# Kernel tuning notes

Measured on AMD Instinct MI355X. Metric: run time of the kernel, lower is better.

The kernel has to match this reference:

```python
import jax, jax.numpy as jnp
import numpy as np

PHI = 1.6
JITTER = 1e-4
ETA = 1.0
BETA = 0.5
EPS_CHOL = 1e-6
R_NEIGH = 2


def _solve3(L, d):
    # lower-triangular 3x3 forward substitution; L broadcasts against d[..., 3]
    y0 = d[..., 0] / L[..., 0, 0]
    y1 = (d[..., 1] - L[..., 1, 0] * y0) / L[..., 1, 1]
    y2 = (d[..., 2] - L[..., 2, 0] * y0 - L[..., 2, 1] * y1) / L[..., 2, 2]
    return jnp.stack([y0, y1, y2], axis=-1)


def _overlap_score(delta, L):
    # fused_gaussian_overlap_score: Gaussian log-overlap ~ -0.5*(Mahalanobis + logdet)
    y = _solve3(L, delta)
    maha = jnp.sum(y * y, axis=-1)
    logdet = 2.0 * jnp.sum(jnp.log(jnp.diagonal(L, axis1=-2, axis2=-1)), axis=-1)
    return -0.5 * (maha + logdet)


def _head(x, ln_g, ln_b, W1, b1, W2, b2):
    # LayerNorm -> Linear -> SiLU -> Linear(->1), squeeze
    m = jnp.mean(x, axis=-1, keepdims=True)
    v = jnp.var(x, axis=-1, keepdims=True)
    h = (x - m) / jnp.sqrt(v + 1e-5) * ln_g + ln_b
    h = jax.nn.silu(h @ W1 + b1)
    return (h @ W2 + b2)[..., 0]


def setup_inputs() -> dict:
    key = jax.random.key(0)
    ks = jax.random.split(key, 12)
    B, Kp, M, C = 2, 1024, 8, 256
    s_parent = jax.random.normal(ks[0], (B, Kp, C), jnp.float32)
    mu_p = jax.random.normal(ks[1], (B, Kp, 3), jnp.float32) * 10.0
    A = jax.random.normal(ks[2], (B, Kp, 3, 3), jnp.float32) * 0.5
    Sigma_p = jnp.einsum('bkij,bklj->bkil', A, A) + 0.05 * jnp.eye(3, dtype=jnp.float32)
    mask_parent = jnp.ones((B, Kp), jnp.float32)
    xi_noise = jax.random.normal(ks[3], (B, Kp, M, 3), jnp.float32)
    emb = jax.random.normal(ks[4], (M, C), jnp.float32) * 0.02
    lin = lambda k, fi, fo, s=0.02: jax.random.normal(k, (fi, fo), jnp.float32) * s
    return dict(
        s_parent=s_parent, mu_p=mu_p, Sigma_p=Sigma_p, mask_parent=mask_parent,
        xi_noise=xi_noise, emb=emb,
        gate_ln_g=jnp.ones((C,), jnp.float32), gate_ln_b=jnp.zeros((C,), jnp.float32),
        gate_W1=lin(ks[5], C, C), gate_b1=jnp.zeros((C,), jnp.float32),
        gate_W2=lin(ks[6], C, 1), gate_b2=jnp.zeros((1,), jnp.float32),
        prior_ln_g=jnp.ones((C,), jnp.float32), prior_ln_b=jnp.zeros((C,), jnp.float32),
        prior_W1=lin(ks[7], C, C), prior_b1=jnp.zeros((C,), jnp.float32),
        prior_W2=lin(ks[8], C, 1), prior_b2=jnp.zeros((1,), jnp.float32),
        geom_W=lin(ks[9], C, 3, 0.01), geom_b=jnp.zeros((3,), jnp.float32),
        K_target=6144,
    )


def reference(s_parent, mu_p, Sigma_p, mask_parent, xi_noise, emb,
              gate_ln_g, gate_ln_b, gate_W1, gate_b1, gate_W2, gate_b2,
              prior_ln_g, prior_ln_b, prior_W1, prior_b1, prior_W2, prior_b2,
              geom_W, geom_b, K_target):
    B, Kp, C = s_parent.shape
    M = emb.shape[0]
    Kc = Kp * M
    I3 = jnp.eye(3, dtype=s_parent.dtype)

    # --- candidate children from per-parent Cholesky splat ---
    Lp = jnp.linalg.cholesky(Sigma_p + EPS_CHOL * I3)               # [B,Kp,3,3]
    xi = xi_noise + (emb @ geom_W + geom_b)                          # [B,Kp,M,3]
    mu0 = mu_p[:, :, None, :] + jnp.einsum('bkae,bkme->bkma', Lp, xi)
    mu0 = mu0.reshape(B, Kc, 3)

    j0 = jnp.repeat(jnp.arange(Kp), M)                               # [Kc] birth parent
    t_ids = jnp.tile(jnp.arange(M), Kp)                              # [Kc] child slot
    m0 = mask_parent[:, j0]

    # --- gate g ---
    gate_in = s_parent[:, j0, :] + emb[t_ids]                        # [B,Kc,C]
    b = _head(gate_in, gate_ln_g, gate_ln_b, gate_W1, gate_b1, gate_W2, gate_b2)
    a = jax.nn.softplus(_head(s_parent, prior_ln_g, prior_ln_b, prior_W1, prior_b1, prior_W2, prior_b2))
    b = b + BETA * jnp.log(a[:, j0] + 1e-8)
    g = jax.nn.sigmoid(b / max(ETA, 1e-6)) * m0                      # [B,Kc]
    loss_count = jnp.mean((jnp.sum(g, axis=1) - float(K_target)) ** 2)

    # --- top-R neighbor parents by overlap score (indices only, no grad) ---
    mu0_birth = mu_p[:, j0, :]                                       # mu of birth parent
    delta1 = mu0_birth[:, :, None, :] - mu_p[:, None, :, :]          # [B,Kc,Kp,3]
    score1 = _overlap_score(delta1, Lp[:, None])                     # [B,Kc,Kp]
    self_hot = (jnp.arange(Kp)[None, :] == j0[:, None])              # [Kc,Kp]
    score1 = jnp.where(self_hot[None], 1e9, score1)
    _, neigh = jax.lax.top_k(jax.lax.stop_gradient(score1), R_NEIGH) # [B,Kc,R], col0=j0

    bidx = jnp.arange(B)[:, None, None]
    mu_nei = mu_p[bidx, neigh]                                       # [B,Kc,R,3]
    Sig_nei = Sigma_p[bidx, neigh]                                   # [B,Kc,R,3,3]
    L_nei = Lp[bidx, neigh]
    s_nei = s_parent[bidx, neigh]                                    # [B,Kc,R,C]

    # --- soft responsibilities over the R neighbors ---
    score2 = _overlap_score(mu0[:, :, None, :] - mu_nei, L_nei)      # [B,Kc,R]
    w = jax.nn.softmax(score2, axis=-1)

    # --- moment-matching refine (sparse form of B_resp: rows of B are w scattered at neigh) ---
    mu_child = jnp.einsum('bir,bird->bid', w, mu_nei)                # [B,Kc,3]
    intra = jnp.einsum('bir,birmn->bimn', w, Sig_nei) * PHI ** (-2)
    dmu = mu_nei - mu_child[:, :, None, :]
    inter = jnp.einsum('bir,birm,birn->bimn', w, dmu, dmu)
    Sigma_child = intra + inter + JITTER * I3                        # [B,Kc,3,3]

    s_mix = jnp.einsum('bir,birc->bic', w, s_nei)
    s_child0 = g[..., None] * s_mix                                  # [B,Kc,C]
    return s_child0, mu_child, Sigma_child, g, loss_count
```

## Files before the change

### kernel.cpp

```cpp
#include <hip/hip_runtime.h>
#include <math.h>

#define NPAR 2048
#define KP   1024
#define MM   8
#define CC   256
#define KC   8192
#define NCH  16384

#define WS_PKL    0
#define WS_PKI    8192
#define WS_PKM    16384
#define WS_L22    24576
#define WS_MEANSP 26624
#define WS_SUMSQ  28672
#define WS_DOT8   30720
#define WS_APRIOR 47104
#define WS_EGATE  49152
#define WS_UGATE  51200
#define WS_C0GATE 51456
#define WS_GEO    51712
#define WS_MEANE  51736
#define WS_SUMSQE 51744
#define WS_NEIGH  51752
#define WS_PGATE  53824

#define OUT_S    0
#define OUT_MU   4194304
#define OUT_SIG  4243456
#define OUT_G    4390912
#define OUT_LOSS 4407296

__device__ __forceinline__ float siluf(float x){ return x / (1.f + expf(-x)); }
__device__ __forceinline__ float softplusf(float x){ return x > 20.f ? x : log1pf(expf(x)); }

__global__ __launch_bounds__(256) void kP1(const float* __restrict__ sp,
                                           const float* __restrict__ mu_p,
                                           const float* __restrict__ Sig,
                                           const float* __restrict__ emb,
                                           const float* __restrict__ geom_W,
                                           const float* __restrict__ geom_b,
                                           float* __restrict__ ws) {
  int blk = blockIdx.x;
  int t = threadIdx.x;
  if (blk < 512) {
    int pid  = blk * 4 + (t >> 6);
    int lane = t & 63;
    const float4 v = *(const float4*)(sp + pid * CC + lane * 4);
    float s  = v.x + v.y + v.z + v.w;
    float ss = v.x*v.x + v.y*v.y + v.z*v.z + v.w*v.w;
    float pd[8];
#pragma unroll
    for (int m = 0; m < 8; m++) {
      float4 e = *(const float4*)(emb + m * CC + lane * 4);
      pd[m] = v.x*e.x + v.y*e.y + v.z*e.z + v.w*e.w;
    }
#pragma unroll
    for (int o = 32; o > 0; o >>= 1) {
      s  += __shfl_xor(s, o);
      ss += __shfl_xor(ss, o);
#pragma unroll
      for (int m = 0; m < 8; m++) pd[m] += __shfl_xor(pd[m], o);
    }
    if (lane == 0) {
      ws[WS_MEANSP + pid] = s * (1.f / 256.f);
      ws[WS_SUMSQ + pid]  = ss;
#pragma unroll
      for (int m = 0; m < 8; m++) ws[WS_DOT8 + pid * 8 + m] = pd[m];
    }
  } else if (blk < 520) {
    int pid = (blk - 512) * 256 + t;
    const float* S = Sig + pid * 9;
    float a00 = S[0] + 1e-6f, a10 = S[3], a11 = S[4] + 1e-6f;
    float a20 = S[6], a21 = S[7], a22 = S[8] + 1e-6f;
    float L00 = sqrtf(a00); float i0 = 1.f / L00;
    float L10 = a10 * i0, L20 = a20 * i0;
    float L11 = sqrtf(a11 - L10 * L10); float i1 = 1.f / L11;
    float L21 = (a21 - L20 * L10) * i1;
    float L22 = sqrtf(a22 - L20 * L20 - L21 * L21); float i2 = 1.f / L22;
    float logdet = 2.f * logf(L00 * L11 * L22);
    float4 pkl = {L10, L20, L21, logdet};
    float4 pki = {i0, i1, i2, L00};
    float4 pkm = {mu_p[pid*3+0], mu_p[pid*3+1], mu_p[pid*3+2], L11};
    *(float4*)(ws + WS_PKL + pid * 4) = pkl;
    *(float4*)(ws + WS_PKI + pid * 4) = pki;
    *(float4*)(ws + WS_PKM + pid * 4) = pkm;
    ws[WS_L22 + pid] = L22;
  } else {
    if (t < 192) {
      int o = t >> 3, lane8 = t & 7;
      int m = o / 3, d = o % 3;
      float acc = 0.f;
      for (int k = lane8; k < 256; k += 8) acc += emb[m * 256 + k] * geom_W[k * 3 + d];
      acc += __shfl_xor(acc, 1); acc += __shfl_xor(acc, 2); acc += __shfl_xor(acc, 4);
      if (lane8 == 0) ws[WS_GEO + o] = acc + geom_b[d];
    } else {
      int o = (t - 192) >> 3, lane8 = t & 7;
      if (o < 8) {
        float s = 0.f, ss = 0.f;
        for (int k = lane8; k < 256; k += 8) { float e = emb[o * 256 + k]; s += e; ss += e * e; }
        s  += __shfl_xor(s, 1);  s  += __shfl_xor(s, 2);  s  += __shfl_xor(s, 4);
        ss += __shfl_xor(ss, 1); ss += __shfl_xor(ss, 2); ss += __shfl_xor(ss, 4);
        if (lane8 == 0) { ws[WS_MEANE + o] = s * (1.f / 256.f); ws[WS_SUMSQE + o] = ss; }
      }
    }
  }
}

__global__ __launch_bounds__(256) void kP2(const float* __restrict__ sp,
                                           const float* __restrict__ emb,
                                           const float* __restrict__ g_ln_g,
                                           const float* __restrict__ g_ln_b,
                                           const float* __restrict__ gW1,
                                           const float* __restrict__ gb1,
                                           const float* __restrict__ p_ln_g,
                                           const float* __restrict__ p_ln_b,
                                           const float* __restrict__ pW1,
                                           const float* __restrict__ pb1,
                                           const float* __restrict__ pW2,
                                           const float* __restrict__ pb2,
                                           float* __restrict__ ws) {
  __shared__ float xs[8][256];
  __shared__ float red[4][8];
  __shared__ float redS[4][8];
  __shared__ float redQ[4][8];
  __shared__ float mv[2][8];
  int blk = blockIdx.x;
  int t = threadIdx.x;

  if (blk < 512) {
    int wv = blk * 4 + (t >> 6);
    int lane = t & 63;
    int b = wv >> 10;
    int j = wv & (KP - 1);
    const float4 qm = *(const float4*)(ws + WS_PKM + wv * 4);
    float qx = qm.x, qy = qm.y, qz = qm.z;
    float best = -3.4e38f; int bidx = 1 << 30;
    for (int it = 0; it < 16; it++) {
      int k = it * 64 + lane;
      int idx = b * KP + k;
      float4 pl = *(const float4*)(ws + WS_PKL + idx * 4);
      float4 pi = *(const float4*)(ws + WS_PKI + idx * 4);
      float4 pm = *(const float4*)(ws + WS_PKM + idx * 4);
      float dx = qx - pm.x, dy = qy - pm.y, dz = qz - pm.z;
      float y0 = dx * pi.x;
      float y1 = (dy - pl.x * y0) * pi.y;
      float y2 = (dz - pl.y * y0 - pl.z * y1) * pi.z;
      float sc = -0.5f * (y0*y0 + y1*y1 + y2*y2 + pl.w);
      if (k == j) sc = -3.4e38f;
      if (sc > best || (sc == best && k < bidx)) { best = sc; bidx = k; }
    }
#pragma unroll
    for (int o = 32; o > 0; o >>= 1) {
      float ob = __shfl_xor(best, o);
      int   oi = __shfl_xor(bidx, o);
      if (ob > best || (ob == best && oi < bidx)) { best = ob; bidx = oi; }
    }
    if (lane == 0) ((int*)ws)[WS_NEIGH + wv] = bidx;
  } else {
    int cblk = blk - 512;
    bool prior = (cblk >= 256 && cblk < 512);
    const float* W1 = prior ? pW1 : gW1;

    if (cblk < 256) {
      int base = cblk * 8;
      float g = g_ln_g[t];
#pragma unroll
      for (int r = 0; r < 8; r++) xs[r][t] = sp[(base + r) * 256 + t] * g;
    } else if (cblk < 512) {
      int base = (cblk - 256) * 8;
      float vr[8], s1[8], s2[8];
#pragma unroll
      for (int r = 0; r < 8; r++) {
        vr[r] = sp[(base + r) * 256 + t];
        s1[r] = vr[r];
        s2[r] = vr[r] * vr[r];
      }
#pragma unroll
      for (int o = 32; o > 0; o >>= 1) {
#pragma unroll
        for (int r = 0; r < 8; r++) { s1[r] += __shfl_xor(s1[r], o); s2[r] += __shfl_xor(s2[r], o); }
      }
      int wave = t >> 6;
      if ((t & 63) == 0) {
#pragma unroll
        for (int r = 0; r < 8; r++) { redS[wave][r] = s1[r]; redQ[wave][r] = s2[r]; }
      }
      __syncthreads();
      if (t < 8) {
        float sum = redS[0][t] + redS[1][t] + redS[2][t] + redS[3][t];
        float sq  = redQ[0][t] + redQ[1][t] + redQ[2][t] + redQ[3][t];
        float mean = sum * (1.f / 256.f);
        float var  = sq * (1.f / 256.f) - mean * mean;
        mv[0][t] = mean;
        mv[1][t] = rsqrtf(var + 1e-5f);
      }
      __syncthreads();
      float pg = p_ln_g[t], pbv = p_ln_b[t];
#pragma unroll
      for (int r = 0; r < 8; r++)
        xs[r][t] = (vr[r] - mv[0][r]) * mv[1][r] * pg + pbv;
    } else if (cblk == 512) {
      float g = g_ln_g[t];
#pragma unroll
      for (int r = 0; r < 8; r++) xs[r][t] = emb[r * 256 + t] * g;
    } else {
      xs[0][t] = g_ln_g[t];
      xs[1][t] = g_ln_b[t];
#pragma unroll
      for (int r = 2; r < 8; r++) xs[r][t] = 0.f;
    }
    __syncthreads();

    float acc[8] = {0,0,0,0,0,0,0,0};
    for (int k4 = 0; k4 < 256; k4 += 4) {
      float w0 = W1[(k4+0) * 256 + t];
      float w1 = W1[(k4+1) * 256 + t];
      float w2 = W1[(k4+2) * 256 + t];
      float w3 = W1[(k4+3) * 256 + t];
#pragma unroll
      for (int r = 0; r < 8; r++) {
        float4 x4 = *(const float4*)&xs[r][k4];
        acc[r] += x4.x * w0 + x4.y * w1 + x4.z * w2 + x4.w * w3;
      }
    }

    if (cblk < 256) {
      int base = cblk * 8;
#pragma unroll
      for (int r = 0; r < 8; r++) ws[WS_PGATE + (base + r) * 256 + t] = acc[r];
    } else if (cblk < 512) {
      int base = (cblk - 256) * 8;
      float b1 = pb1[t], w2 = pW2[t];
      float tv[8];
#pragma unroll
      for (int r = 0; r < 8; r++) {
        float h = acc[r] + b1;
        tv[r] = siluf(h) * w2;
      }
#pragma unroll
      for (int o = 32; o > 0; o >>= 1) {
#pragma unroll
        for (int r = 0; r < 8; r++) tv[r] += __shfl_xor(tv[r], o);
      }
      int wave = t >> 6;
      if ((t & 63) == 0) {
#pragma unroll
        for (int r = 0; r < 8; r++) red[wave][r] = tv[r];
      }
      __syncthreads();
      if (t < 8) {
        float sum = red[0][t] + red[1][t] + red[2][t] + red[3][t] + pb2[0];
        ws[WS_APRIOR + base + t] = softplusf(sum);
      }
    } else if (cblk == 512) {
#pragma unroll
      for (int r = 0; r < 8; r++) ws[WS_EGATE + r * 256 + t] = acc[r];
    } else {
      ws[WS_UGATE + t]  = acc[0];
      ws[WS_C0GATE + t] = acc[1] + gb1[t];
    }
  }
}

__global__ __launch_bounds__(256) void kD(const float* __restrict__ sp,
                                          const float* __restrict__ Sig,
                                          const float* __restrict__ mask,
                                          const float* __restrict__ xi_noise,
                                          const float* __restrict__ gW2,
                                          const float* __restrict__ gb2,
                                          const float* __restrict__ ws,
                                          float* __restrict__ out) {
  int wv   = blockIdx.x * 4 + (threadIdx.x >> 6);
  int lane = threadIdx.x & 63;
  int b = wv >> 13;
  int i = wv & (KC - 1);
  int j = i >> 3;
  int m = i & 7;
  int prow = b * KP + j;

  float mean_x = ws[WS_MEANSP + prow] + ws[WS_MEANE + m];
  float Ex2 = ws[WS_SUMSQ + prow] + 2.f * ws[WS_DOT8 + prow * 8 + m] + ws[WS_SUMSQE + m];
  float var = Ex2 * (1.f / 256.f) - mean_x * mean_x;
  float rstd = rsqrtf(var + 1e-5f);

  int c4 = lane * 4;
  float Pv[4], Ev[4], Uv[4], C0v[4], W2v[4];
  *(float4*)Pv  = *(const float4*)(ws + WS_PGATE + prow * 256 + c4);
  *(float4*)Ev  = *(const float4*)(ws + WS_EGATE + m * 256 + c4);
  *(float4*)Uv  = *(const float4*)(ws + WS_UGATE + c4);
  *(float4*)C0v = *(const float4*)(ws + WS_C0GATE + c4);
  *(float4*)W2v = *(const float4*)(gW2 + c4);
  float partial = 0.f;
#pragma unroll
  for (int q = 0; q < 4; q++) {
    float pre = (Pv[q] + Ev[q] - mean_x * Uv[q]) * rstd + C0v[q];
    partial += siluf(pre) * W2v[q];
  }
#pragma unroll
  for (int o = 32; o > 0; o >>= 1) partial += __shfl_xor(partial, o);
  float aP = ws[WS_APRIOR + prow];
  float bval = partial + gb2[0] + 0.5f * logf(aP + 1e-8f);
  float g = (1.f / (1.f + expf(-bval))) * mask[prow];

  const float4 plP = *(const float4*)(ws + WS_PKL + prow * 4);
  const float4 piP = *(const float4*)(ws + WS_PKI + prow * 4);
  const float4 pmP = *(const float4*)(ws + WS_PKM + prow * 4);
  float L22 = ws[WS_L22 + prow];

  int xbase = (prow * 8 + m) * 3;
  float x0 = xi_noise[xbase + 0] + ws[WS_GEO + m * 3 + 0];
  float x1 = xi_noise[xbase + 1] + ws[WS_GEO + m * 3 + 1];
  float x2 = xi_noise[xbase + 2] + ws[WS_GEO + m * 3 + 2];
  float m0x = pmP.x + piP.w * x0;
  float m0y = pmP.y + plP.x * x0 + pmP.w * x1;
  float m0z = pmP.z + plP.y * x0 + plP.z * x1 + L22 * x2;

  int n1 = ((const int*)ws)[WS_NEIGH + prow];
  int nrow1 = b * KP + n1;
  const float4 plN = *(const float4*)(ws + WS_PKL + nrow1 * 4);
  const float4 piN = *(const float4*)(ws + WS_PKI + nrow1 * 4);
  const float4 pmN = *(const float4*)(ws + WS_PKM + nrow1 * 4);

  float sc[2], nx[2], ny[2], nz[2];
  {
    float dx = m0x - pmP.x, dy = m0y - pmP.y, dz = m0z - pmP.z;
    float y0 = dx * piP.x;
    float y1 = (dy - plP.x * y0) * piP.y;
    float y2 = (dz - plP.y * y0 - plP.z * y1) * piP.z;
    sc[0] = -0.5f * (y0*y0 + y1*y1 + y2*y2 + plP.w);
    nx[0] = pmP.x; ny[0] = pmP.y; nz[0] = pmP.z;
  }
  {
    float dx = m0x - pmN.x, dy = m0y - pmN.y, dz = m0z - pmN.z;
    float y0 = dx * piN.x;
    float y1 = (dy - plN.x * y0) * piN.y;
    float y2 = (dz - plN.y * y0 - plN.z * y1) * piN.z;
    sc[1] = -0.5f * (y0*y0 + y1*y1 + y2*y2 + plN.w);
    nx[1] = pmN.x; ny[1] = pmN.y; nz[1] = pmN.z;
  }
  float mxs = fmaxf(sc[0], sc[1]);
  float e0 = expf(sc[0] - mxs), e1 = expf(sc[1] - mxs);
  float inv = 1.f / (e0 + e1);
  float w0 = e0 * inv, w1 = e1 * inv;

  float mcx = w0 * nx[0] + w1 * nx[1];
  float mcy = w0 * ny[0] + w1 * ny[1];
  float mcz = w0 * nz[0] + w1 * nz[1];

  float d0x = nx[0] - mcx, d0y = ny[0] - mcy, d0z = nz[0] - mcz;
  float d1x = nx[1] - mcx, d1y = ny[1] - mcy, d1z = nz[1] - mcz;
  const float* S0 = Sig + prow * 9;
  const float* S1 = Sig + nrow1 * 9;
  const float PHIm2 = 0.390625f;
  float Sout[9];
  float dd0[3] = {d0x, d0y, d0z};
  float dd1[3] = {d1x, d1y, d1z};
#pragma unroll
  for (int a = 0; a < 3; a++)
#pragma unroll
    for (int e = 0; e < 3; e++) {
      float v = (w0 * S0[a*3+e] + w1 * S1[a*3+e]) * PHIm2
              + w0 * dd0[a] * dd0[e] + w1 * dd1[a] * dd1[e];
      if (a == e) v += 1e-4f;
      Sout[a*3+e] = v;
    }

  if (lane == 0) {
    float* om = out + OUT_MU + wv * 3;
    om[0] = mcx; om[1] = mcy; om[2] = mcz;
    out[OUT_G + wv] = g;
    float* os = out + OUT_SIG + wv * 9;
#pragma unroll
    for (int q = 0; q < 9; q++) os[q] = Sout[q];
  }

  float s0v[4], s1v[4], ov[4];
  *(float4*)s0v = *(const float4*)(sp + prow * 256 + c4);
  *(float4*)s1v = *(const float4*)(sp + nrow1 * 256 + c4);
  float gw0 = g * w0, gw1 = g * w1;
#pragma unroll
  for (int q = 0; q < 4; q++) ov[q] = gw0 * s0v[q] + gw1 * s1v[q];
  *(float4*)(out + OUT_S + wv * 256 + c4) = *(float4*)ov;
}

__global__ __launch_bounds__(256) void kF(const float* __restrict__ out_in,
                                          const int* __restrict__ Kt,
                                          float* __restrict__ out) {
  __shared__ float red[4][2];
  int t = threadIdx.x;
  const float* gp = out_in + OUT_G;
  float s0 = 0.f, s1 = 0.f;
  for (int it = 0; it < 32; it++) {
    s0 += gp[it * 256 + t];
    s1 += gp[KC + it * 256 + t];
  }
#pragma unroll
  for (int o = 32; o > 0; o >>= 1) {
    s0 += __shfl_xor(s0, o);
    s1 += __shfl_xor(s1, o);
  }
  int wave = t >> 6;
  if ((t & 63) == 0) { red[wave][0] = s0; red[wave][1] = s1; }
  __syncthreads();
  if (t == 0) {
    float S0 = red[0][0] + red[1][0] + red[2][0] + red[3][0];
    float S1 = red[0][1] + red[1][1] + red[2][1] + red[3][1];
    float K = (float)Kt[0];
    float l0 = S0 - K, l1 = S1 - K;
    out[OUT_LOSS] = 0.5f * (l0 * l0 + l1 * l1);
  }
}

extern "C" void kernel_launch(void* const* d_in, const int* in_sizes, int n_in,
                              void* d_out, int out_size, void* d_ws, size_t ws_size,
                              hipStream_t stream) {
  const float* s_parent   = (const float*)d_in[0];
  const float* mu_p       = (const float*)d_in[1];
  const float* Sigma_p    = (const float*)d_in[2];
  const float* mask_par   = (const float*)d_in[3];
  const float* xi_noise   = (const float*)d_in[4];
  const float* emb        = (const float*)d_in[5];
  const float* gate_ln_g  = (const float*)d_in[6];
  const float* gate_ln_b  = (const float*)d_in[7];
  const float* gate_W1    = (const float*)d_in[8];
  const float* gate_b1    = (const float*)d_in[9];
  const float* gate_W2    = (const float*)d_in[10];
  const float* gate_b2    = (const float*)d_in[11];
  const float* prior_ln_g = (const float*)d_in[12];
  const float* prior_ln_b = (const float*)d_in[13];
  const float* prior_W1   = (const float*)d_in[14];
  const float* prior_b1   = (const float*)d_in[15];
  const float* prior_W2   = (const float*)d_in[16];
  const float* prior_b2   = (const float*)d_in[17];
  const float* geom_W     = (const float*)d_in[18];
  const float* geom_b     = (const float*)d_in[19];
  const int*   K_target   = (const int*)d_in[20];

  float* ws  = (float*)d_ws;
  float* out = (float*)d_out;

  kP1<<<521, 256, 0, stream>>>(s_parent, mu_p, Sigma_p, emb, geom_W, geom_b, ws);
  kP2<<<1026, 256, 0, stream>>>(s_parent, emb, gate_ln_g, gate_ln_b, gate_W1, gate_b1,
                                prior_ln_g, prior_ln_b, prior_W1, prior_b1,
                                prior_W2, prior_b2, ws);
  kD<<<NCH / 4, 256, 0, stream>>>(s_parent, Sigma_p, mask_par, xi_noise,
                                  gate_W2, gate_b2, ws, out);
  kF<<<1, 256, 0, stream>>>(out, K_target, out);
}
```

Measured before the change: 146.2 us.

## Fold LayerNorm gains into W1 and share one GEMM pass for gate and prior

```diff
diff --git a/kernel.cpp b/kernel.cpp
--- a/kernel.cpp
+++ b/kernel.cpp
@@ -24,6 +24,11 @@
 #define WS_SUMSQE 51744
 #define WS_NEIGH  51752
 #define WS_PGATE  53824
+#define WS_WI     578112
+#define WS_UGP    709184
+#define WS_C0GP   711232
+#define WS_UPP    713280
+#define WS_C0PP   715328
 
 #define OUT_S    0
 #define OUT_MU   4194304
@@ -40,6 +45,12 @@
                                            const float* __restrict__ emb,
                                            const float* __restrict__ geom_W,
                                            const float* __restrict__ geom_b,
+                                           const float* __restrict__ g_ln_g,
+                                           const float* __restrict__ g_ln_b,
+                                           const float* __restrict__ gW1,
+                                           const float* __restrict__ p_ln_g,
+                                           const float* __restrict__ p_ln_b,
+                                           const float* __restrict__ pW1,
                                            float* __restrict__ ws) {
   int blk = blockIdx.x;
   int t = threadIdx.x;
@@ -86,7 +97,7 @@
     *(float4*)(ws + WS_PKI + pid * 4) = pki;
     *(float4*)(ws + WS_PKM + pid * 4) = pkm;
     ws[WS_L22 + pid] = L22;
-  } else {
+  } else if (blk == 520) {
     if (t < 192) {
       int o = t >> 3, lane8 = t & 7;
       int m = o / 3, d = o % 3;
@@ -104,27 +115,38 @@
         if (lane8 == 0) { ws[WS_MEANE + o] = s * (1.f / 256.f); ws[WS_SUMSQE + o] = ss; }
       }
     }
+  } else {
+    int q = blk - 521;
+    float2* WI = (float2*)(ws + WS_WI);
+    float pug = 0.f, pc0g = 0.f, pup = 0.f, pc0p = 0.f;
+    for (int kk = 0; kk < 32; kk++) {
+      int k = q * 32 + kk;
+      float lg = g_ln_g[k], lbg = g_ln_b[k];
+      float lp = p_ln_g[k], lbp = p_ln_b[k];
+      float gv = gW1[k * 256 + t];
+      float pv = pW1[k * 256 + t];
+      float wg = lg * gv, wp = lp * pv;
+      float2 wi = {wg, wp};
+      WI[k * 256 + t] = wi;
+      pug  += wg;         pc0g += lbg * gv;
+      pup  += wp;         pc0p += lbp * pv;
+    }
+    ws[WS_UGP  + q * 256 + t] = pug;
+    ws[WS_C0GP + q * 256 + t] = pc0g;
+    ws[WS_UPP  + q * 256 + t] = pup;
+    ws[WS_C0PP + q * 256 + t] = pc0p;
   }
 }
 
 __global__ __launch_bounds__(256) void kP2(const float* __restrict__ sp,
                                            const float* __restrict__ emb,
-                                           const float* __restrict__ g_ln_g,
-                                           const float* __restrict__ g_ln_b,
-                                           const float* __restrict__ gW1,
                                            const float* __restrict__ gb1,
-                                           const float* __restrict__ p_ln_g,
-                                           const float* __restrict__ p_ln_b,
-                                           const float* __restrict__ pW1,
                                            const float* __restrict__ pb1,
                                            const float* __restrict__ pW2,
                                            const float* __restrict__ pb2,
                                            float* __restrict__ ws) {
   __shared__ float xs[8][256];
   __shared__ float red[4][8];
-  __shared__ float redS[4][8];
-  __shared__ float redQ[4][8];
-  __shared__ float mv[2][8];
   int blk = blockIdx.x;
   int t = threadIdx.x;
 
@@ -157,109 +179,95 @@
       if (ob > best || (ob == best && oi < bidx)) { best = ob; bidx = oi; }
     }
     if (lane == 0) ((int*)ws)[WS_NEIGH + wv] = bidx;
+  } else if (blk < 769) {
+    bool isE = (blk == 768);
+    int cblk = blk - 512;
+    int base = cblk * 8;
+    const float2* WI = (const float2*)(ws + WS_WI);
+
+    if (isE) {
+#pragma unroll
+      for (int r = 0; r < 8; r++) xs[r][t] = emb[r * 256 + t];
+    } else {
+#pragma unroll
+      for (int r = 0; r < 8; r++) xs[r][t] = sp[(base + r) * 256 + t];
+    }
+    __syncthreads();
+
+    float accg[8] = {0,0,0,0,0,0,0,0};
+    float accp[8] = {0,0,0,0,0,0,0,0};
+    float2 wnext[8];
+#pragma unroll
+    for (int i = 0; i < 8; i++) wnext[i] = WI[i * 256 + t];
+    for (int kb = 0; kb < 256; kb += 8) {
+      float2 wc[8];
+#pragma unroll
+      for (int i = 0; i < 8; i++) wc[i] = wnext[i];
+      if (kb + 8 < 256) {
+#pragma unroll
+        for (int i = 0; i < 8; i++) wnext[i] = WI[(kb + 8 + i) * 256 + t];
+      }
+#pragma unroll
+      for (int i = 0; i < 8; i += 4) {
+#pragma unroll
+        for (int r = 0; r < 8; r++) {
+          float4 x = *(const float4*)&xs[r][kb + i];
+          accg[r] += x.x * wc[i].x + x.y * wc[i+1].x + x.z * wc[i+2].x + x.w * wc[i+3].x;
+          accp[r] += x.x * wc[i].y + x.y * wc[i+1].y + x.z * wc[i+2].y + x.w * wc[i+3].y;
+        }
+      }
+    }
+
+    if (isE) {
+#pragma unroll
+      for (int r = 0; r < 8; r++) ws[WS_EGATE + r * 256 + t] = accg[r];
+      return;
+    }
+
+#pragma unroll
+    for (int r = 0; r < 8; r++) ws[WS_PGATE + (base + r) * 256 + t] = accg[r];
+
+    float up = 0.f, c0p = 0.f;
+#pragma unroll
+    for (int q = 0; q < 8; q++) {
+      up  += ws[WS_UPP  + q * 256 + t];
+      c0p += ws[WS_C0PP + q * 256 + t];
+    }
+    c0p += pb1[t];
+    float w2 = pW2[t];
+    float tv[8];
+#pragma unroll
+    for (int r = 0; r < 8; r++) {
+      float mean = ws[WS_MEANSP + base + r];
+      float var  = ws[WS_SUMSQ + base + r] * (1.f / 256.f) - mean * mean;
+      float rstd = rsqrtf(var + 1e-5f);
+      float h = (accp[r] - mean * up) * rstd + c0p;
+      tv[r] = siluf(h) * w2;
+    }
+#pragma unroll
+    for (int o = 32; o > 0; o >>= 1) {
+#pragma unroll
+      for (int r = 0; r < 8; r++) tv[r] += __shfl_xor(tv[r], o);
+    }
+    int wave = t >> 6;
+    if ((t & 63) == 0) {
+#pragma unroll
+      for (int r = 0; r < 8; r++) red[wave][r] = tv[r];
+    }
+    __syncthreads();
+    if (t < 8) {
+      float sum = red[0][t] + red[1][t] + red[2][t] + red[3][t] + pb2[0];
+      ws[WS_APRIOR + base + t] = softplusf(sum);
+    }
   } else {
-    int cblk = blk - 512;
-    bool prior = (cblk >= 256 && cblk < 512);
-    const float* W1 = prior ? pW1 : gW1;
-
-    if (cblk < 256) {
-      int base = cblk * 8;
-      float g = g_ln_g[t];
-#pragma unroll
-      for (int r = 0; r < 8; r++) xs[r][t] = sp[(base + r) * 256 + t] * g;
-    } else if (cblk < 512) {
-      int base = (cblk - 256) * 8;
-      float vr[8], s1[8], s2[8];
-#pragma unroll
-      for (int r = 0; r < 8; r++) {
-        vr[r] = sp[(base + r) * 256 + t];
-        s1[r] = vr[r];
-        s2[r] = vr[r] * vr[r];
-      }
-#pragma unroll
-      for (int o = 32; o > 0; o >>= 1) {
-#pragma unroll
-        for (int r = 0; r < 8; r++) { s1[r] += __shfl_xor(s1[r], o); s2[r] += __shfl_xor(s2[r], o); }
-      }
-      int wave = t >> 6;
-      if ((t & 63) == 0) {
-#pragma unroll
-        for (int r = 0; r < 8; r++) { redS[wave][r] = s1[r]; redQ[wave][r] = s2[r]; }
-      }
-      __syncthreads();
-      if (t < 8) {
-        float sum = redS[0][t] + redS[1][t] + redS[2][t] + redS[3][t];
-        float sq  = redQ[0][t] + redQ[1][t] + redQ[2][t] + redQ[3][t];
-        float mean = sum * (1.f / 256.f);
-        float var  = sq * (1.f / 256.f) - mean * mean;
-        mv[0][t] = mean;
-        mv[1][t] = rsqrtf(var + 1e-5f);
-      }
-      __syncthreads();
-      float pg = p_ln_g[t], pbv = p_ln_b[t];
-#pragma unroll
-      for (int r = 0; r < 8; r++)
-        xs[r][t] = (vr[r] - mv[0][r]) * mv[1][r] * pg + pbv;
-    } else if (cblk == 512) {
-      float g = g_ln_g[t];
-#pragma unroll
-      for (int r = 0; r < 8; r++) xs[r][t] = emb[r * 256 + t] * g;
-    } else {
-      xs[0][t] = g_ln_g[t];
-      xs[1][t] = g_ln_b[t];
-#pragma unroll
-      for (int r = 2; r < 8; r++) xs[r][t] = 0.f;
-    }
-    __syncthreads();
-
-    float acc[8] = {0,0,0,0,0,0,0,0};
-    for (int k4 = 0; k4 < 256; k4 += 4) {
-      float w0 = W1[(k4+0) * 256 + t];
-      float w1 = W1[(k4+1) * 256 + t];
-      float w2 = W1[(k4+2) * 256 + t];
-      float w3 = W1[(k4+3) * 256 + t];
-#pragma unroll
-      for (int r = 0; r < 8; r++) {
-        float4 x4 = *(const float4*)&xs[r][k4];
-        acc[r] += x4.x * w0 + x4.y * w1 + x4.z * w2 + x4.w * w3;
-      }
-    }
-
-    if (cblk < 256) {
-      int base = cblk * 8;
-#pragma unroll
-      for (int r = 0; r < 8; r++) ws[WS_PGATE + (base + r) * 256 + t] = acc[r];
-    } else if (cblk < 512) {
-      int base = (cblk - 256) * 8;
-      float b1 = pb1[t], w2 = pW2[t];
-      float tv[8];
-#pragma unroll
-      for (int r = 0; r < 8; r++) {
-        float h = acc[r] + b1;
-        tv[r] = siluf(h) * w2;
-      }
-#pragma unroll
-      for (int o = 32; o > 0; o >>= 1) {
-#pragma unroll
-        for (int r = 0; r < 8; r++) tv[r] += __shfl_xor(tv[r], o);
-      }
-      int wave = t >> 6;
-      if ((t & 63) == 0) {
-#pragma unroll
-        for (int r = 0; r < 8; r++) red[wave][r] = tv[r];
-      }
-      __syncthreads();
-      if (t < 8) {
-        float sum = red[0][t] + red[1][t] + red[2][t] + red[3][t] + pb2[0];
-        ws[WS_APRIOR + base + t] = softplusf(sum);
-      }
-    } else if (cblk == 512) {
-#pragma unroll
-      for (int r = 0; r < 8; r++) ws[WS_EGATE + r * 256 + t] = acc[r];
-    } else {
-      ws[WS_UGATE + t]  = acc[0];
-      ws[WS_C0GATE + t] = acc[1] + gb1[t];
-    }
+    float ug = 0.f, c0g = 0.f;
+#pragma unroll
+    for (int q = 0; q < 8; q++) {
+      ug  += ws[WS_UGP  + q * 256 + t];
+      c0g += ws[WS_C0GP + q * 256 + t];
+    }
+    ws[WS_UGATE + t]  = ug;
+    ws[WS_C0GATE + t] = c0g + gb1[t];
   }
 }
 
@@ -440,10 +448,11 @@
   float* ws  = (float*)d_ws;
   float* out = (float*)d_out;
 
-  kP1<<<521, 256, 0, stream>>>(s_parent, mu_p, Sigma_p, emb, geom_W, geom_b, ws);
-  kP2<<<1026, 256, 0, stream>>>(s_parent, emb, gate_ln_g, gate_ln_b, gate_W1, gate_b1,
-                                prior_ln_g, prior_ln_b, prior_W1, prior_b1,
-                                prior_W2, prior_b2, ws);
+  kP1<<<529, 256, 0, stream>>>(s_parent, mu_p, Sigma_p, emb, geom_W, geom_b,
+                               gate_ln_g, gate_ln_b, gate_W1,
+                               prior_ln_g, prior_ln_b, prior_W1, ws);
+  kP2<<<770, 256, 0, stream>>>(s_parent, emb, gate_b1, prior_b1,
+                               prior_W2, prior_b2, ws);
   kD<<<NCH / 4, 256, 0, stream>>>(s_parent, Sigma_p, mask_par, xi_noise,
                                   gate_W2, gate_b2, ws, out);
   kF<<<1, 256, 0, stream>>>(out, K_target, out);
```

Result: slower. 154.9 us (+5.9%).

## Double rows per GEMM block, prefetch weights, fold prior LayerNorm algebraically

Applied to the files above, without the earlier changes.

```diff
diff --git a/kernel.cpp b/kernel.cpp
--- a/kernel.cpp
+++ b/kernel.cpp
@@ -33,6 +33,31 @@
 
 __device__ __forceinline__ float siluf(float x){ return x / (1.f + expf(-x)); }
 __device__ __forceinline__ float softplusf(float x){ return x > 20.f ? x : log1pf(expf(x)); }
+
+template<int NR>
+__device__ __forceinline__ void gemm_k(const float* __restrict__ W1, int t,
+                                       const float xs[][256], float* acc) {
+  float wn[8];
+#pragma unroll
+  for (int i = 0; i < 8; i++) wn[i] = W1[i * 256 + t];
+  for (int kb = 0; kb < 256; kb += 8) {
+    float wc[8];
+#pragma unroll
+    for (int i = 0; i < 8; i++) wc[i] = wn[i];
+    if (kb + 8 < 256) {
+#pragma unroll
+      for (int i = 0; i < 8; i++) wn[i] = W1[(kb + 8 + i) * 256 + t];
+    }
+#pragma unroll
+    for (int i = 0; i < 8; i += 4) {
+#pragma unroll
+      for (int r = 0; r < NR; r++) {
+        float4 x = *(const float4*)&xs[r][kb + i];
+        acc[r] += x.x * wc[i] + x.y * wc[i+1] + x.z * wc[i+2] + x.w * wc[i+3];
+      }
+    }
+  }
+}
 
 __global__ __launch_bounds__(256) void kP1(const float* __restrict__ sp,
                                            const float* __restrict__ mu_p,
@@ -120,11 +145,8 @@
                                            const float* __restrict__ pW2,
                                            const float* __restrict__ pb2,
                                            float* __restrict__ ws) {
-  __shared__ float xs[8][256];
-  __shared__ float red[4][8];
-  __shared__ float redS[4][8];
-  __shared__ float redQ[4][8];
-  __shared__ float mv[2][8];
+  __shared__ float xs[18][256];
+  __shared__ float red[4][16];
   int blk = blockIdx.x;
   int t = threadIdx.x;
 
@@ -157,109 +179,73 @@
       if (ob > best || (ob == best && oi < bidx)) { best = ob; bidx = oi; }
     }
     if (lane == 0) ((int*)ws)[WS_NEIGH + wv] = bidx;
+  } else if (blk < 640) {
+    int base = (blk - 512) * 16;
+    float lg = g_ln_g[t];
+#pragma unroll
+    for (int r = 0; r < 16; r++) xs[r][t] = sp[(base + r) * 256 + t] * lg;
+    __syncthreads();
+    float acc[16];
+#pragma unroll
+    for (int r = 0; r < 16; r++) acc[r] = 0.f;
+    gemm_k<16>(gW1, t, xs, acc);
+#pragma unroll
+    for (int r = 0; r < 16; r++) ws[WS_PGATE + (base + r) * 256 + t] = acc[r];
+  } else if (blk < 768) {
+    int base = (blk - 640) * 16;
+    float lp = p_ln_g[t];
+#pragma unroll
+    for (int r = 0; r < 16; r++) xs[r][t] = sp[(base + r) * 256 + t] * lp;
+    xs[16][t] = lp;
+    xs[17][t] = p_ln_b[t];
+    __syncthreads();
+    float acc[18];
+#pragma unroll
+    for (int r = 0; r < 18; r++) acc[r] = 0.f;
+    gemm_k<18>(pW1, t, xs, acc);
+
+    float up  = acc[16];
+    float c0p = acc[17] + pb1[t];
+    float w2 = pW2[t];
+    float tv[16];
+#pragma unroll
+    for (int r = 0; r < 16; r++) {
+      float mean = ws[WS_MEANSP + base + r];
+      float var  = ws[WS_SUMSQ + base + r] * (1.f / 256.f) - mean * mean;
+      float rstd = rsqrtf(var + 1e-5f);
+      float h = (acc[r] - mean * up) * rstd + c0p;
+      tv[r] = siluf(h) * w2;
+    }
+#pragma unroll
+    for (int o = 32; o > 0; o >>= 1) {
+#pragma unroll
+      for (int r = 0; r < 16; r++) tv[r] += __shfl_xor(tv[r], o);
+    }
+    int wave = t >> 6;
+    if ((t & 63) == 0) {
+#pragma unroll
+      for (int r = 0; r < 16; r++) red[wave][r] = tv[r];
+    }
+    __syncthreads();
+    if (t < 16) {
+      float sum = red[0][t] + red[1][t] + red[2][t] + red[3][t] + pb2[0];
+      ws[WS_APRIOR + base + t] = softplusf(sum);
+    }
   } else {
-    int cblk = blk - 512;
-    bool prior = (cblk >= 256 && cblk < 512);
-    const float* W1 = prior ? pW1 : gW1;
-
-    if (cblk < 256) {
-      int base = cblk * 8;
-      float g = g_ln_g[t];
-#pragma unroll
-      for (int r = 0; r < 8; r++) xs[r][t] = sp[(base + r) * 256 + t] * g;
-    } else if (cblk < 512) {
-      int base = (cblk - 256) * 8;
-      float vr[8], s1[8], s2[8];
-#pragma unroll
-      for (int r = 0; r < 8; r++) {
-        vr[r] = sp[(base + r) * 256 + t];
-        s1[r] = vr[r];
-        s2[r] = vr[r] * vr[r];
-      }
-#pragma unroll
-      for (int o = 32; o > 0; o >>= 1) {
-#pragma unroll
-        for (int r = 0; r < 8; r++) { s1[r] += __shfl_xor(s1[r], o); s2[r] += __shfl_xor(s2[r], o); }
-      }
-      int wave = t >> 6;
-      if ((t & 63) == 0) {
-#pragma unroll
-        for (int r = 0; r < 8; r++) { redS[wave][r] = s1[r]; redQ[wave][r] = s2[r]; }
-      }
-      __syncthreads();
-      if (t < 8) {
-        float sum = redS[0][t] + redS[1][t] + redS[2][t] + redS[3][t];
-        float sq  = redQ[0][t] + redQ[1][t] + redQ[2][t] + redQ[3][t];
-        float mean = sum * (1.f / 256.f);
-        float var  = sq * (1.f / 256.f) - mean * mean;
-        mv[0][t] = mean;
-        mv[1][t] = rsqrtf(var + 1e-5f);
-      }
-      __syncthreads();
-      float pg = p_ln_g[t], pbv = p_ln_b[t];
-#pragma unroll
-      for (int r = 0; r < 8; r++)
-        xs[r][t] = (vr[r] - mv[0][r]) * mv[1][r] * pg + pbv;
-    } else if (cblk == 512) {
-      float g = g_ln_g[t];
-#pragma unroll
-      for (int r = 0; r < 8; r++) xs[r][t] = emb[r * 256 + t] * g;
-    } else {
-      xs[0][t] = g_ln_g[t];
-      xs[1][t] = g_ln_b[t];
-#pragma unroll
-      for (int r = 2; r < 8; r++) xs[r][t] = 0.f;
-    }
+    float lg = g_ln_g[t];
+#pragma unroll
+    for (int r = 0; r < 8; r++) xs[r][t] = emb[r * 256 + t] * lg;
+    xs[8][t] = lg;
+    xs[9][t] = g_ln_b[t];
     __syncthreads();
-
-    float acc[8] = {0,0,0,0,0,0,0,0};
-    for (int k4 = 0; k4 < 256; k4 += 4) {
-      float w0 = W1[(k4+0) * 256 + t];
-      float w1 = W1[(k4+1) * 256 + t];
-      float w2 = W1[(k4+2) * 256 + t];
-      float w3 = W1[(k4+3) * 256 + t];
-#pragma unroll
-      for (int r = 0; r < 8; r++) {
-        float4 x4 = *(const float4*)&xs[r][k4];
-        acc[r] += x4.x * w0 + x4.y * w1 + x4.z * w2 + x4.w * w3;
-      }
-    }
-
-    if (cblk < 256) {
-      int base = cblk * 8;
-#pragma unroll
-      for (int r = 0; r < 8; r++) ws[WS_PGATE + (base + r) * 256 + t] = acc[r];
-    } else if (cblk < 512) {
-      int base = (cblk - 256) * 8;
-      float b1 = pb1[t], w2 = pW2[t];
-      float tv[8];
-#pragma unroll
-      for (int r = 0; r < 8; r++) {
-        float h = acc[r] + b1;
-        tv[r] = siluf(h) * w2;
-      }
-#pragma unroll
-      for (int o = 32; o > 0; o >>= 1) {
-#pragma unroll
-        for (int r = 0; r < 8; r++) tv[r] += __shfl_xor(tv[r], o);
-      }
-      int wave = t >> 6;
-      if ((t & 63) == 0) {
-#pragma unroll
-        for (int r = 0; r < 8; r++) red[wave][r] = tv[r];
-      }
-      __syncthreads();
-      if (t < 8) {
-        float sum = red[0][t] + red[1][t] + red[2][t] + red[3][t] + pb2[0];
-        ws[WS_APRIOR + base + t] = softplusf(sum);
-      }
-    } else if (cblk == 512) {
-#pragma unroll
-      for (int r = 0; r < 8; r++) ws[WS_EGATE + r * 256 + t] = acc[r];
-    } else {
-      ws[WS_UGATE + t]  = acc[0];
-      ws[WS_C0GATE + t] = acc[1] + gb1[t];
-    }
+    float acc[10];
+#pragma unroll
+    for (int r = 0; r < 10; r++) acc[r] = 0.f;
+    gemm_k<10>(gW1, t, xs, acc);
+#pragma unroll
+    for (int r = 0; r < 8; r++) ws[WS_EGATE + r * 256 + t] = acc[r];
+    ws[WS_UGATE + t]  = acc[8];
+    ws[WS_C0GATE + t] = acc[9] + gb1[t];
   }
 }
 
@@ -441,9 +427,9 @@
   float* out = (float*)d_out;
 
   kP1<<<521, 256, 0, stream>>>(s_parent, mu_p, Sigma_p, emb, geom_W, geom_b, ws);
-  kP2<<<1026, 256, 0, stream>>>(s_parent, emb, gate_ln_g, gate_ln_b, gate_W1, gate_b1,
-                                prior_ln_g, prior_ln_b, prior_W1, prior_b1,
-                                prior_W2, prior_b2, ws);
+  kP2<<<769, 256, 0, stream>>>(s_parent, emb, gate_ln_g, gate_ln_b, gate_W1, gate_b1,
+                               prior_ln_g, prior_ln_b, prior_W1, prior_b1,
+                               prior_W2, prior_b2, ws);
   kD<<<NCH / 4, 256, 0, stream>>>(s_parent, Sigma_p, mask_par, xi_noise,
                                   gate_W2, gate_b2, ws, out);
   kF<<<1, 256, 0, stream>>>(out, K_target, out);
```

Measured after the change: 163.2 us. 11.6% more time.
